# Performance work log

Measured on AMD Instinct MI355X. Metric: run time of the kernel, lower is better.

Reference implementation:

```python
import jax, jax.numpy as jnp
import numpy as np

WINDOW_SIZE = 11
CHANNEL = 3
SIGMA = 1.5
C1 = 0.01 ** 2
C2 = 0.03 ** 2


def _make_window():
    coords = jnp.arange(WINDOW_SIZE, dtype=jnp.float32) - WINDOW_SIZE // 2
    g = jnp.exp(-coords ** 2 / (2 * SIGMA ** 2))
    g = g / g.sum()
    w2d = jnp.outer(g, g)                      # (K, K)
    # (C, 1, K, K) depthwise kernel, OIHW with feature_group_count=C
    return jnp.broadcast_to(w2d[None, None], (CHANNEL, 1, WINDOW_SIZE, WINDOW_SIZE))


def _dwconv(x, w):
    # x: (1, C, H, W), w: (C, 1, K, K) -> same-padded depthwise conv
    pad = WINDOW_SIZE // 2
    return jax.lax.conv_general_dilated(
        x, w, window_strides=(1, 1), padding=[(pad, pad), (pad, pad)],
        feature_group_count=CHANNEL,
        dimension_numbers=('NCHW', 'OIHW', 'NCHW'))


def setup_inputs() -> dict:
    key = jax.random.key(0)
    k1, k2 = jax.random.split(key)
    H = W = 2048
    img1 = jax.random.uniform(k1, (H, W, 3), dtype=jnp.float32)
    img2 = jax.random.uniform(k2, (H, W, 3), dtype=jnp.float32)
    window = _make_window()
    return {"img1": img1, "img2": img2, "window": window}


def reference(img1, img2, window):
    # (H, W, C) -> (1, C, H, W)
    x = jnp.transpose(img1, (2, 0, 1))[None]
    y = jnp.transpose(img2, (2, 0, 1))[None]

    mu1 = _dwconv(x, window)
    mu2 = _dwconv(y, window)
    mu1_sq = mu1 ** 2
    mu2_sq = mu2 ** 2
    mu12 = mu1 * mu2

    sigma1_sq = _dwconv(x * x, window) - mu1_sq
    sigma2_sq = _dwconv(y * y, window) - mu2_sq
    sigma12 = _dwconv(x * y, window) - mu12

    ssim_map = ((2 * mu12 + C1) * (2 * sigma12 + C2)) / (
        (mu1_sq + mu2_sq + C1) * (sigma1_sq + sigma2_sq + C2))
    return 1.0 - ssim_map.mean()
```

## Files before the change

kernel.cpp:

```cpp
#include <hip/hip_runtime.h>
#include <math.h>

#define TILE_W 32
#define TILE_H 16
#define HALO 5
#define IH   26
#define LDSW 44
#define HBW  36

__global__ void zero_kernel(float* ws) { ws[0] = 0.0f; }

__global__ void finalize_kernel(const float* ws, float* out, float inv_n) {
    out[0] = 1.0f - ws[0] * inv_n;
}

__global__ void reduce_kernel(const float* __restrict__ ws, float* __restrict__ out,
                              int n, float inv_n) {
    __shared__ float s[16];
    float a = 0.0f;
    for (int i = threadIdx.x; i < n; i += 1024) a += ws[i];
    #pragma unroll
    for (int off = 32; off > 0; off >>= 1) a += __shfl_down(a, off, 64);
    if ((threadIdx.x & 63) == 0) s[threadIdx.x >> 6] = a;
    __syncthreads();
    if (threadIdx.x == 0) {
        float t = 0.0f;
        #pragma unroll
        for (int w = 0; w < 16; ++w) t += s[w];
        out[0] = 1.0f - t * inv_n;
    }
}

__global__ __launch_bounds__(256, 4) void ssim_kernel(
    const float* __restrict__ img1, const float* __restrict__ img2,
    const float* __restrict__ window, float* __restrict__ ws,
    int H, int W, int use_partials)
{
    __shared__ float sx[IH][LDSW];
    __shared__ float sy[IH][LDSW];
    __shared__ float hb[5][IH][HBW];
    __shared__ float wsum[4];

    const int tid = threadIdx.x;
    const int x0  = blockIdx.x * TILE_W;
    const int y0  = blockIdx.y * TILE_H;
    const int c   = blockIdx.z;

    float gr[11];
    {
        float inv = 1.0f / sqrtf(window[60]);
        #pragma unroll
        for (int t = 0; t < 11; ++t) gr[t] = window[55 + t] * inv;
    }

    const bool interior = (x0 >= HALO) && (x0 + 39 <= W) &&
                          (y0 >= HALO) && (y0 + 21 <= H);

    float acc = 0.0f;

    if (interior) {
        for (int item = tid; item < IH * 11; item += 256) {
            int r   = item / 11;
            int j4  = (item % 11) * 4;
            long base = ((long)(y0 + r - HALO) * W + (x0 + j4 - HALO)) * 3 + c;
            float vx[4], vy[4];
            #pragma unroll
            for (int k = 0; k < 4; ++k) {
                vx[k] = img1[base + 3 * k];
                vy[k] = img2[base + 3 * k];
            }
            *(float4*)&sx[r][j4] = make_float4(vx[0], vx[1], vx[2], vx[3]);
            *(float4*)&sy[r][j4] = make_float4(vy[0], vy[1], vy[2], vy[3]);
        }
    } else {
        for (int item = tid; item < IH * 11; item += 256) {
            int r   = item / 11;
            int j4  = (item % 11) * 4;
            int gh  = y0 + r - HALO;
            int gx0 = x0 + j4 - HALO;
            bool rowok = ((unsigned)gh < (unsigned)H);
            float vx[4], vy[4];
            #pragma unroll
            for (int k = 0; k < 4; ++k) {
                int gx = gx0 + k;
                bool ok = rowok && ((unsigned)gx < (unsigned)W);
                long off = ((long)gh * W + gx) * 3 + c;
                vx[k] = ok ? img1[off] : 0.0f;
                vy[k] = ok ? img2[off] : 0.0f;
            }
            *(float4*)&sx[r][j4] = make_float4(vx[0], vx[1], vx[2], vx[3]);
            *(float4*)&sy[r][j4] = make_float4(vy[0], vy[1], vy[2], vy[3]);
        }
    }
    __syncthreads();

    if (tid < IH * 8) {
        int r  = tid >> 3;
        int j4 = (tid & 7) * 4;
        float xv[16], yv[16];
        *(float4*)&xv[0]  = *(const float4*)&sx[r][j4];
        *(float4*)&xv[4]  = *(const float4*)&sx[r][j4 + 4];
        *(float4*)&xv[8]  = *(const float4*)&sx[r][j4 + 8];
        *(float4*)&xv[12] = *(const float4*)&sx[r][j4 + 12];
        *(float4*)&yv[0]  = *(const float4*)&sy[r][j4];
        *(float4*)&yv[4]  = *(const float4*)&sy[r][j4 + 4];
        *(float4*)&yv[8]  = *(const float4*)&sy[r][j4 + 8];
        *(float4*)&yv[12] = *(const float4*)&sy[r][j4 + 12];

        float h0[4] = {0,0,0,0}, h1[4] = {0,0,0,0}, h2[4] = {0,0,0,0};
        float h3[4] = {0,0,0,0}, h4[4] = {0,0,0,0};
        #pragma unroll
        for (int t = 0; t < 14; ++t) {
            float xs = xv[t] * xv[t];
            float ys = yv[t] * yv[t];
            float xy = xv[t] * yv[t];
            #pragma unroll
            for (int jj = 0; jj < 4; ++jj) {
                int k = t - jj;
                if (k >= 0 && k <= 10) {
                    float g = gr[k];
                    h0[jj] += g * xv[t];
                    h1[jj] += g * yv[t];
                    h2[jj] += g * xs;
                    h3[jj] += g * ys;
                    h4[jj] += g * xy;
                }
            }
        }
        *(float4*)&hb[0][r][j4] = make_float4(h0[0], h0[1], h0[2], h0[3]);
        *(float4*)&hb[1][r][j4] = make_float4(h1[0], h1[1], h1[2], h1[3]);
        *(float4*)&hb[2][r][j4] = make_float4(h2[0], h2[1], h2[2], h2[3]);
        *(float4*)&hb[3][r][j4] = make_float4(h3[0], h3[1], h3[2], h3[3]);
        *(float4*)&hb[4][r][j4] = make_float4(h4[0], h4[1], h4[2], h4[3]);
    }
    __syncthreads();

    {
        int j  = tid & 31;
        int i0 = (tid >> 5) * 2;
        float m1[2]  = {0,0}, m2[2]  = {0,0};
        float v11[2] = {0,0}, v22[2] = {0,0}, v12[2] = {0,0};
        #pragma unroll
        for (int t = 0; t < 12; ++t) {
            float b0 = hb[0][i0 + t][j];
            float b1 = hb[1][i0 + t][j];
            float b2 = hb[2][i0 + t][j];
            float b3 = hb[3][i0 + t][j];
            float b4 = hb[4][i0 + t][j];
            #pragma unroll
            for (int o = 0; o < 2; ++o) {
                int k = t - o;
                if (k >= 0 && k <= 10) {
                    float g = gr[k];
                    m1[o]  += g * b0;
                    m2[o]  += g * b1;
                    v11[o] += g * b2;
                    v22[o] += g * b3;
                    v12[o] += g * b4;
                }
            }
        }
        const float C1 = 0.0001f, C2 = 0.0009f;
        #pragma unroll
        for (int o = 0; o < 2; ++o) {
            int gy = y0 + i0 + o, gx = x0 + j;
            if (gy < H && gx < W) {
                float mu1 = m1[o], mu2 = m2[o];
                float mu11 = mu1 * mu1, mu22 = mu2 * mu2, mu12 = mu1 * mu2;
                float s11 = v11[o] - mu11;
                float s22 = v22[o] - mu22;
                float s12 = v12[o] - mu12;
                float num = (2.0f * mu12 + C1) * (2.0f * s12 + C2);
                float den = (mu11 + mu22 + C1) * (s11 + s22 + C2);
                acc += num / den;
            }
        }
    }

    #pragma unroll
    for (int off = 32; off > 0; off >>= 1)
        acc += __shfl_down(acc, off, 64);
    int lane = tid & 63, wid = tid >> 6;
    if (lane == 0) wsum[wid] = acc;
    __syncthreads();
    if (tid == 0) {
        float total = wsum[0] + wsum[1] + wsum[2] + wsum[3];
        if (use_partials)
            ws[(blockIdx.z * gridDim.y + blockIdx.y) * gridDim.x + blockIdx.x] = total;
        else
            atomicAdd(ws, total);
    }
}

extern "C" void kernel_launch(void* const* d_in, const int* in_sizes, int n_in,
                              void* d_out, int out_size, void* d_ws, size_t ws_size,
                              hipStream_t stream) {
    const float* img1   = (const float*)d_in[0];
    const float* img2   = (const float*)d_in[1];
    const float* window = (const float*)d_in[2];
    float* out = (float*)d_out;
    float* ws  = (float*)d_ws;

    long hw = (long)in_sizes[0] / 3;
    int W = (int)(sqrt((double)hw) + 0.5);
    int H = (int)(hw / W);

    float inv_n = (float)(1.0 / ((double)H * (double)W * 3.0));

    dim3 grid((W + TILE_W - 1) / TILE_W, (H + TILE_H - 1) / TILE_H, 3);
    long nblocks = (long)grid.x * grid.y * grid.z;
    int use_partials = (ws_size >= (size_t)nblocks * sizeof(float)) ? 1 : 0;

    if (use_partials) {
        ssim_kernel<<<grid, 256, 0, stream>>>(img1, img2, window, ws, H, W, 1);
        reduce_kernel<<<1, 1024, 0, stream>>>(ws, out, (int)nblocks, inv_n);
    } else {
        zero_kernel<<<1, 1, 0, stream>>>(ws);
        ssim_kernel<<<grid, 256, 0, stream>>>(img1, img2, window, ws, H, W, 0);
        finalize_kernel<<<1, 1, 0, stream>>>(ws, out, inv_n);
    }
}
```

Baseline: 226.2 us.

## Alias LDS buffers, interleave channels in grid, and widen vertical pass per thread

The input tiles and the horizontal-pass buffer now share one LDS union, cutting shared memory per block so more blocks can be resident per CU. Horizontal results are kept in registers across an extra barrier before being written over the input tiles. Channel is folded into blockIdx.x so the three channel blocks for a tile run next to each other and share cache lines of the interleaved RGB input. The vertical pass uses 128 threads computing 4 outputs each, which reuses loaded rows but idles half the block. The divide becomes a hardware reciprocal, trading a little precision for speed.

```diff
diff --git a/kernel.cpp b/kernel.cpp
--- a/kernel.cpp
+++ b/kernel.cpp
@@ -36,15 +36,17 @@
     const float* __restrict__ window, float* __restrict__ ws,
     int H, int W, int use_partials)
 {
-    __shared__ float sx[IH][LDSW];
-    __shared__ float sy[IH][LDSW];
-    __shared__ float hb[5][IH][HBW];
+    __shared__ union {
+        struct { float sx[IH][LDSW]; float sy[IH][LDSW]; } in;
+        float hb[5][IH][HBW];
+    } u;
     __shared__ float wsum[4];
 
     const int tid = threadIdx.x;
-    const int x0  = blockIdx.x * TILE_W;
+    const int bx  = blockIdx.x;
+    const int c   = bx % 3;
+    const int x0  = (bx / 3) * TILE_W;
     const int y0  = blockIdx.y * TILE_H;
-    const int c   = blockIdx.z;
 
     float gr[11];
     {
@@ -69,8 +71,8 @@
                 vx[k] = img1[base + 3 * k];
                 vy[k] = img2[base + 3 * k];
             }
-            *(float4*)&sx[r][j4] = make_float4(vx[0], vx[1], vx[2], vx[3]);
-            *(float4*)&sy[r][j4] = make_float4(vy[0], vy[1], vy[2], vy[3]);
+            *(float4*)&u.in.sx[r][j4] = make_float4(vx[0], vx[1], vx[2], vx[3]);
+            *(float4*)&u.in.sy[r][j4] = make_float4(vy[0], vy[1], vy[2], vy[3]);
         }
     } else {
         for (int item = tid; item < IH * 11; item += 256) {
@@ -88,27 +90,27 @@
                 vx[k] = ok ? img1[off] : 0.0f;
                 vy[k] = ok ? img2[off] : 0.0f;
             }
-            *(float4*)&sx[r][j4] = make_float4(vx[0], vx[1], vx[2], vx[3]);
-            *(float4*)&sy[r][j4] = make_float4(vy[0], vy[1], vy[2], vy[3]);
-        }
-    }
-    __syncthreads();
-
+            *(float4*)&u.in.sx[r][j4] = make_float4(vx[0], vx[1], vx[2], vx[3]);
+            *(float4*)&u.in.sy[r][j4] = make_float4(vy[0], vy[1], vy[2], vy[3]);
+        }
+    }
+    __syncthreads();
+
+    float h0[4] = {0,0,0,0}, h1[4] = {0,0,0,0}, h2[4] = {0,0,0,0};
+    float h3[4] = {0,0,0,0}, h4[4] = {0,0,0,0};
+    int r_b  = tid >> 3;
+    int j4_b = (tid & 7) * 4;
     if (tid < IH * 8) {
-        int r  = tid >> 3;
-        int j4 = (tid & 7) * 4;
         float xv[16], yv[16];
-        *(float4*)&xv[0]  = *(const float4*)&sx[r][j4];
-        *(float4*)&xv[4]  = *(const float4*)&sx[r][j4 + 4];
-        *(float4*)&xv[8]  = *(const float4*)&sx[r][j4 + 8];
-        *(float4*)&xv[12] = *(const float4*)&sx[r][j4 + 12];
-        *(float4*)&yv[0]  = *(const float4*)&sy[r][j4];
-        *(float4*)&yv[4]  = *(const float4*)&sy[r][j4 + 4];
-        *(float4*)&yv[8]  = *(const float4*)&sy[r][j4 + 8];
-        *(float4*)&yv[12] = *(const float4*)&sy[r][j4 + 12];
-
-        float h0[4] = {0,0,0,0}, h1[4] = {0,0,0,0}, h2[4] = {0,0,0,0};
-        float h3[4] = {0,0,0,0}, h4[4] = {0,0,0,0};
+        *(float4*)&xv[0]  = *(const float4*)&u.in.sx[r_b][j4_b];
+        *(float4*)&xv[4]  = *(const float4*)&u.in.sx[r_b][j4_b + 4];
+        *(float4*)&xv[8]  = *(const float4*)&u.in.sx[r_b][j4_b + 8];
+        *(float4*)&xv[12] = *(const float4*)&u.in.sx[r_b][j4_b + 12];
+        *(float4*)&yv[0]  = *(const float4*)&u.in.sy[r_b][j4_b];
+        *(float4*)&yv[4]  = *(const float4*)&u.in.sy[r_b][j4_b + 4];
+        *(float4*)&yv[8]  = *(const float4*)&u.in.sy[r_b][j4_b + 8];
+        *(float4*)&yv[12] = *(const float4*)&u.in.sy[r_b][j4_b + 12];
+
         #pragma unroll
         for (int t = 0; t < 14; ++t) {
             float xs = xv[t] * xv[t];
@@ -127,28 +129,32 @@
                 }
             }
         }
-        *(float4*)&hb[0][r][j4] = make_float4(h0[0], h0[1], h0[2], h0[3]);
-        *(float4*)&hb[1][r][j4] = make_float4(h1[0], h1[1], h1[2], h1[3]);
-        *(float4*)&hb[2][r][j4] = make_float4(h2[0], h2[1], h2[2], h2[3]);
-        *(float4*)&hb[3][r][j4] = make_float4(h3[0], h3[1], h3[2], h3[3]);
-        *(float4*)&hb[4][r][j4] = make_float4(h4[0], h4[1], h4[2], h4[3]);
-    }
-    __syncthreads();
-
-    {
+    }
+    __syncthreads();
+
+    if (tid < IH * 8) {
+        *(float4*)&u.hb[0][r_b][j4_b] = make_float4(h0[0], h0[1], h0[2], h0[3]);
+        *(float4*)&u.hb[1][r_b][j4_b] = make_float4(h1[0], h1[1], h1[2], h1[3]);
+        *(float4*)&u.hb[2][r_b][j4_b] = make_float4(h2[0], h2[1], h2[2], h2[3]);
+        *(float4*)&u.hb[3][r_b][j4_b] = make_float4(h3[0], h3[1], h3[2], h3[3]);
+        *(float4*)&u.hb[4][r_b][j4_b] = make_float4(h4[0], h4[1], h4[2], h4[3]);
+    }
+    __syncthreads();
+
+    if (tid < 128) {
         int j  = tid & 31;
-        int i0 = (tid >> 5) * 2;
-        float m1[2]  = {0,0}, m2[2]  = {0,0};
-        float v11[2] = {0,0}, v22[2] = {0,0}, v12[2] = {0,0};
-        #pragma unroll
-        for (int t = 0; t < 12; ++t) {
-            float b0 = hb[0][i0 + t][j];
-            float b1 = hb[1][i0 + t][j];
-            float b2 = hb[2][i0 + t][j];
-            float b3 = hb[3][i0 + t][j];
-            float b4 = hb[4][i0 + t][j];
-            #pragma unroll
-            for (int o = 0; o < 2; ++o) {
+        int i0 = (tid >> 5) * 4;
+        float m1[4]  = {0,0,0,0}, m2[4]  = {0,0,0,0};
+        float v11[4] = {0,0,0,0}, v22[4] = {0,0,0,0}, v12[4] = {0,0,0,0};
+        #pragma unroll
+        for (int t = 0; t < 14; ++t) {
+            float b0 = u.hb[0][i0 + t][j];
+            float b1 = u.hb[1][i0 + t][j];
+            float b2 = u.hb[2][i0 + t][j];
+            float b3 = u.hb[3][i0 + t][j];
+            float b4 = u.hb[4][i0 + t][j];
+            #pragma unroll
+            for (int o = 0; o < 4; ++o) {
                 int k = t - o;
                 if (k >= 0 && k <= 10) {
                     float g = gr[k];
@@ -162,7 +168,7 @@
         }
         const float C1 = 0.0001f, C2 = 0.0009f;
         #pragma unroll
-        for (int o = 0; o < 2; ++o) {
+        for (int o = 0; o < 4; ++o) {
             int gy = y0 + i0 + o, gx = x0 + j;
             if (gy < H && gx < W) {
                 float mu1 = m1[o], mu2 = m2[o];
@@ -172,7 +178,7 @@
                 float s12 = v12[o] - mu12;
                 float num = (2.0f * mu12 + C1) * (2.0f * s12 + C2);
                 float den = (mu11 + mu22 + C1) * (s11 + s22 + C2);
-                acc += num / den;
+                acc += num * __builtin_amdgcn_rcpf(den);
             }
         }
     }
@@ -186,7 +192,7 @@
     if (tid == 0) {
         float total = wsum[0] + wsum[1] + wsum[2] + wsum[3];
         if (use_partials)
-            ws[(blockIdx.z * gridDim.y + blockIdx.y) * gridDim.x + blockIdx.x] = total;
+            ws[blockIdx.y * gridDim.x + blockIdx.x] = total;
         else
             atomicAdd(ws, total);
     }
@@ -207,8 +213,10 @@
 
     float inv_n = (float)(1.0 / ((double)H * (double)W * 3.0));
 
-    dim3 grid((W + TILE_W - 1) / TILE_W, (H + TILE_H - 1) / TILE_H, 3);
-    long nblocks = (long)grid.x * grid.y * grid.z;
+    int tiles_x = (W + TILE_W - 1) / TILE_W;
+    int tiles_y = (H + TILE_H - 1) / TILE_H;
+    dim3 grid(tiles_x * 3, tiles_y);
+    long nblocks = (long)grid.x * grid.y;
     int use_partials = (ws_size >= (size_t)nblocks * sizeof(float)) ? 1 : 0;
 
     if (use_partials) {
```

Measured after the change: 234.6 us. 3.7% more time.

## Stream rows through register-resident vertical convolution with interleaved-channel column tiles

Applied to the files above, without the earlier changes.

Replaces the per-channel 2D tile kernel with one in which each thread owns a column of the interleaved HWC float array, streams down the rows and keeps a rolling set of 11 vertical accumulators per statistic in registers. Each finished vertical row goes to a double-buffered LDS plane, and one wavefront per row applies the horizontal pass with stride 3 and computes SSIM. The aim is coalesced loads of all three channels, no strided per-channel gathers, and far less halo reloading. In exchange it adds a __syncthreads per row, leaves only one wave busy during each horizontal step, raises register pressure (55 accumulators) and uses an approximate reciprocal.

```diff
diff --git a/kernel.cpp b/kernel.cpp
--- a/kernel.cpp
+++ b/kernel.cpp
@@ -1,12 +1,10 @@
 #include <hip/hip_runtime.h>
 #include <math.h>
 
-#define TILE_W 32
-#define TILE_H 16
-#define HALO 5
-#define IH   26
-#define LDSW 44
-#define HBW  36
+#define TH     32
+#define NSTEP  (TH + 10)
+#define WIDTH  226
+#define LPLANE 288
 
 __global__ void zero_kernel(float* ws) { ws[0] = 0.0f; }
 
@@ -31,20 +29,23 @@
     }
 }
 
-__global__ __launch_bounds__(256, 4) void ssim_kernel(
+__global__ __launch_bounds__(256, 3) void ssim_kernel(
     const float* __restrict__ img1, const float* __restrict__ img2,
     const float* __restrict__ window, float* __restrict__ ws,
     int H, int W, int use_partials)
 {
-    __shared__ float sx[IH][LDSW];
-    __shared__ float sy[IH][LDSW];
-    __shared__ float hb[5][IH][HBW];
+    __shared__ float vh[2][5][LPLANE];
     __shared__ float wsum[4];
 
-    const int tid = threadIdx.x;
-    const int x0  = blockIdx.x * TILE_W;
-    const int y0  = blockIdx.y * TILE_H;
-    const int c   = blockIdx.z;
+    const int tid  = threadIdx.x;
+    const int lane = tid & 63;
+    const int wid  = tid >> 6;
+    const int W3   = 3 * W;
+
+    const int Fo0 = WIDTH * blockIdx.x;
+    const int Fb  = Fo0 - 15;
+    const int Fv  = Fb + tid;
+    const int r0  = blockIdx.y * TH;
 
     float gr[11];
     {
@@ -53,140 +54,140 @@
         for (int t = 0; t < 11; ++t) gr[t] = window[55 + t] * inv;
     }
 
-    const bool interior = (x0 >= HALO) && (x0 + 39 <= W) &&
-                          (y0 >= HALO) && (y0 + 21 <= H);
-
-    float acc = 0.0f;
-
-    if (interior) {
-        for (int item = tid; item < IH * 11; item += 256) {
-            int r   = item / 11;
-            int j4  = (item % 11) * 4;
-            long base = ((long)(y0 + r - HALO) * W + (x0 + j4 - HALO)) * 3 + c;
-            float vx[4], vy[4];
-            #pragma unroll
-            for (int k = 0; k < 4; ++k) {
-                vx[k] = img1[base + 3 * k];
-                vy[k] = img2[base + 3 * k];
-            }
-            *(float4*)&sx[r][j4] = make_float4(vx[0], vx[1], vx[2], vx[3]);
-            *(float4*)&sy[r][j4] = make_float4(vy[0], vy[1], vy[2], vy[3]);
+    const bool colok = (Fv >= 0) && (Fv < W3);
+
+    const int c    = lane % 3;
+    const int pg   = lane / 3;
+    const int p0   = Fo0 / 3;
+    const int ofo3 = Fo0 - 3 * p0;
+    const int p    = p0 + 4 * pg;
+    const int bidx = 12 * pg + c - ofo3 + 4;
+    const int fo_end = (Fo0 + WIDTH < W3) ? (Fo0 + WIDTH) : W3;
+
+    float acc[5][11];
+    #pragma unroll
+    for (int q = 0; q < 5; ++q)
+        #pragma unroll
+        for (int s = 0; s < 11; ++s) acc[q][s] = 0.0f;
+
+    float ssum = 0.0f;
+
+    const float* p1 = img1 + (long)(r0 - 5) * W3 + Fv;
+    const float* p2 = img2 + (long)(r0 - 5) * W3 + Fv;
+
+    float xpf = 0.0f, ypf = 0.0f;
+    if (colok && (r0 - 5) >= 0 && (r0 - 5) < H) { xpf = *p1; ypf = *p2; }
+
+    #pragma unroll
+    for (int k = 0; k < 10; ++k) {
+        float xc = xpf, yc = ypf;
+        p1 += W3; p2 += W3;
+        int rn = r0 - 4 + k;
+        xpf = 0.0f; ypf = 0.0f;
+        if (colok && rn >= 0 && rn < H) { xpf = *p1; ypf = *p2; }
+
+        float xx = xc * xc, yy = yc * yc, xy = xc * yc;
+        #pragma unroll
+        for (int s = 0; s <= k; ++s) {
+            float g = gr[k - s];
+            acc[0][s] += g * xc;
+            acc[1][s] += g * yc;
+            acc[2][s] += g * xx;
+            acc[3][s] += g * yy;
+            acc[4][s] += g * xy;
         }
-    } else {
-        for (int item = tid; item < IH * 11; item += 256) {
-            int r   = item / 11;
-            int j4  = (item % 11) * 4;
-            int gh  = y0 + r - HALO;
-            int gx0 = x0 + j4 - HALO;
-            bool rowok = ((unsigned)gh < (unsigned)H);
-            float vx[4], vy[4];
-            #pragma unroll
-            for (int k = 0; k < 4; ++k) {
-                int gx = gx0 + k;
-                bool ok = rowok && ((unsigned)gx < (unsigned)W);
-                long off = ((long)gh * W + gx) * 3 + c;
-                vx[k] = ok ? img1[off] : 0.0f;
-                vy[k] = ok ? img2[off] : 0.0f;
-            }
-            *(float4*)&sx[r][j4] = make_float4(vx[0], vx[1], vx[2], vx[3]);
-            *(float4*)&sy[r][j4] = make_float4(vy[0], vy[1], vy[2], vy[3]);
-        }
-    }
-    __syncthreads();
-
-    if (tid < IH * 8) {
-        int r  = tid >> 3;
-        int j4 = (tid & 7) * 4;
-        float xv[16], yv[16];
-        *(float4*)&xv[0]  = *(const float4*)&sx[r][j4];
-        *(float4*)&xv[4]  = *(const float4*)&sx[r][j4 + 4];
-        *(float4*)&xv[8]  = *(const float4*)&sx[r][j4 + 8];
-        *(float4*)&xv[12] = *(const float4*)&sx[r][j4 + 12];
-        *(float4*)&yv[0]  = *(const float4*)&sy[r][j4];
-        *(float4*)&yv[4]  = *(const float4*)&sy[r][j4 + 4];
-        *(float4*)&yv[8]  = *(const float4*)&sy[r][j4 + 8];
-        *(float4*)&yv[12] = *(const float4*)&sy[r][j4 + 12];
-
-        float h0[4] = {0,0,0,0}, h1[4] = {0,0,0,0}, h2[4] = {0,0,0,0};
-        float h3[4] = {0,0,0,0}, h4[4] = {0,0,0,0};
-        #pragma unroll
-        for (int t = 0; t < 14; ++t) {
-            float xs = xv[t] * xv[t];
-            float ys = yv[t] * yv[t];
-            float xy = xv[t] * yv[t];
-            #pragma unroll
-            for (int jj = 0; jj < 4; ++jj) {
-                int k = t - jj;
-                if (k >= 0 && k <= 10) {
-                    float g = gr[k];
-                    h0[jj] += g * xv[t];
-                    h1[jj] += g * yv[t];
-                    h2[jj] += g * xs;
-                    h3[jj] += g * ys;
-                    h4[jj] += g * xy;
+    }
+
+    for (int kb = 10; kb < NSTEP; kb += 11) {
+        #pragma unroll
+        for (int u = 0; u < 11; ++u) {
+            int k = kb + u;
+            if (k < NSTEP) {
+                float xc = xpf, yc = ypf;
+                p1 += W3; p2 += W3;
+                int rn = r0 - 4 + k;
+                xpf = 0.0f; ypf = 0.0f;
+                if (colok && rn >= 0 && rn < H) { xpf = *p1; ypf = *p2; }
+
+                float xx = xc * xc, yy = yc * yc, xy = xc * yc;
+                #pragma unroll
+                for (int s = 0; s < 11; ++s) {
+                    float g = gr[(u + 10 - s) % 11];
+                    acc[0][s] += g * xc;
+                    acc[1][s] += g * yc;
+                    acc[2][s] += g * xx;
+                    acc[3][s] += g * yy;
+                    acc[4][s] += g * xy;
+                }
+
+                float* vb = &vh[k & 1][0][0];
+                vb[0 * LPLANE + tid + 4] = acc[0][u];
+                vb[1 * LPLANE + tid + 4] = acc[1][u];
+                vb[2 * LPLANE + tid + 4] = acc[2][u];
+                vb[3 * LPLANE + tid + 4] = acc[3][u];
+                vb[4 * LPLANE + tid + 4] = acc[4][u];
+                acc[0][u] = 0.0f; acc[1][u] = 0.0f; acc[2][u] = 0.0f;
+                acc[3][u] = 0.0f; acc[4][u] = 0.0f;
+                __syncthreads();
+
+                if (wid == (k & 3) && lane < 60) {
+                    const float* rb = vb + bidx;
+                    float h0[4] = {0,0,0,0}, h1[4] = {0,0,0,0},
+                          h2[4] = {0,0,0,0}, h3[4] = {0,0,0,0},
+                          h4[4] = {0,0,0,0};
+                    #pragma unroll
+                    for (int t = 0; t < 14; ++t) {
+                        float b0 = rb[0 * LPLANE + 3 * t];
+                        float b1 = rb[1 * LPLANE + 3 * t];
+                        float b2 = rb[2 * LPLANE + 3 * t];
+                        float b3 = rb[3 * LPLANE + 3 * t];
+                        float b4 = rb[4 * LPLANE + 3 * t];
+                        #pragma unroll
+                        for (int i = 0; i < 4; ++i) {
+                            int s = t - i;
+                            if (s >= 0 && s <= 10) {
+                                float g = gr[s];
+                                h0[i] += g * b0;
+                                h1[i] += g * b1;
+                                h2[i] += g * b2;
+                                h3[i] += g * b3;
+                                h4[i] += g * b4;
+                            }
+                        }
+                    }
+                    int o = r0 + k - 10;
+                    if (o < H) {
+                        const float C1 = 0.0001f, C2 = 0.0009f;
+                        #pragma unroll
+                        for (int i = 0; i < 4; ++i) {
+                            int fo = 3 * (p + i) + c;
+                            if (fo >= Fo0 && fo < fo_end) {
+                                float mu1 = h0[i], mu2 = h1[i];
+                                float mu11 = mu1 * mu1, mu22 = mu2 * mu2;
+                                float mu12 = mu1 * mu2;
+                                float s11 = h2[i] - mu11;
+                                float s22 = h3[i] - mu22;
+                                float s12 = h4[i] - mu12;
+                                float num = (2.0f * mu12 + C1) * (2.0f * s12 + C2);
+                                float den = (mu11 + mu22 + C1) * (s11 + s22 + C2);
+                                ssum += num * __builtin_amdgcn_rcpf(den);
+                            }
+                        }
+                    }
                 }
             }
         }
-        *(float4*)&hb[0][r][j4] = make_float4(h0[0], h0[1], h0[2], h0[3]);
-        *(float4*)&hb[1][r][j4] = make_float4(h1[0], h1[1], h1[2], h1[3]);
-        *(float4*)&hb[2][r][j4] = make_float4(h2[0], h2[1], h2[2], h2[3]);
-        *(float4*)&hb[3][r][j4] = make_float4(h3[0], h3[1], h3[2], h3[3]);
-        *(float4*)&hb[4][r][j4] = make_float4(h4[0], h4[1], h4[2], h4[3]);
-    }
-    __syncthreads();
-
-    {
-        int j  = tid & 31;
-        int i0 = (tid >> 5) * 2;
-        float m1[2]  = {0,0}, m2[2]  = {0,0};
-        float v11[2] = {0,0}, v22[2] = {0,0}, v12[2] = {0,0};
-        #pragma unroll
-        for (int t = 0; t < 12; ++t) {
-            float b0 = hb[0][i0 + t][j];
-            float b1 = hb[1][i0 + t][j];
-            float b2 = hb[2][i0 + t][j];
-            float b3 = hb[3][i0 + t][j];
-            float b4 = hb[4][i0 + t][j];
-            #pragma unroll
-            for (int o = 0; o < 2; ++o) {
-                int k = t - o;
-                if (k >= 0 && k <= 10) {
-                    float g = gr[k];
-                    m1[o]  += g * b0;
-                    m2[o]  += g * b1;
-                    v11[o] += g * b2;
-                    v22[o] += g * b3;
-                    v12[o] += g * b4;
-                }
-            }
-        }
-        const float C1 = 0.0001f, C2 = 0.0009f;
-        #pragma unroll
-        for (int o = 0; o < 2; ++o) {
-            int gy = y0 + i0 + o, gx = x0 + j;
-            if (gy < H && gx < W) {
-                float mu1 = m1[o], mu2 = m2[o];
-                float mu11 = mu1 * mu1, mu22 = mu2 * mu2, mu12 = mu1 * mu2;
-                float s11 = v11[o] - mu11;
-                float s22 = v22[o] - mu22;
-                float s12 = v12[o] - mu12;
-                float num = (2.0f * mu12 + C1) * (2.0f * s12 + C2);
-                float den = (mu11 + mu22 + C1) * (s11 + s22 + C2);
-                acc += num / den;
-            }
-        }
     }
 
     #pragma unroll
     for (int off = 32; off > 0; off >>= 1)
-        acc += __shfl_down(acc, off, 64);
-    int lane = tid & 63, wid = tid >> 6;
-    if (lane == 0) wsum[wid] = acc;
+        ssum += __shfl_down(ssum, off, 64);
+    if (lane == 0) wsum[wid] = ssum;
     __syncthreads();
     if (tid == 0) {
         float total = wsum[0] + wsum[1] + wsum[2] + wsum[3];
         if (use_partials)
-            ws[(blockIdx.z * gridDim.y + blockIdx.y) * gridDim.x + blockIdx.x] = total;
+            ws[blockIdx.y * gridDim.x + blockIdx.x] = total;
         else
             atomicAdd(ws, total);
     }
@@ -207,8 +208,10 @@
 
     float inv_n = (float)(1.0 / ((double)H * (double)W * 3.0));
 
-    dim3 grid((W + TILE_W - 1) / TILE_W, (H + TILE_H - 1) / TILE_H, 3);
-    long nblocks = (long)grid.x * grid.y * grid.z;
+    int gx = (3 * W + WIDTH - 1) / WIDTH;
+    int gy = (H + TH - 1) / TH;
+    dim3 grid(gx, gy);
+    long nblocks = (long)gx * gy;
     int use_partials = (ws_size >= (size_t)nblocks * sizeof(float)) ? 1 : 0;
 
     if (use_partials) {
```

New measurement: 297.5 us. 1.32x slower.
